# Kernel optimization log

Hardware: AMD Instinct MI355X
Metric: run time of the kernel (lower is better)

Reference implementation:

```python
import jax, jax.numpy as jnp
import numpy as np

VOCAB = 32000
EMB = 512
STATE = 512
B = 4
S = 1024


def setup_inputs() -> dict:
    key = jax.random.key(0)
    ks = jax.random.split(key, 6)
    x = jax.random.randint(ks[0], (B, S), 0, VOCAB)
    emb_table = jax.random.normal(ks[1], (VOCAB, EMB), dtype=jnp.float32)
    a = jax.random.normal(ks[2], (STATE, STATE), dtype=jnp.float32) * 0.02
    b = jax.random.normal(ks[3], (EMB, STATE), dtype=jnp.float32) * 0.02
    # nn.Linear(state, vocab): weight [vocab, state], bias [vocab]
    lim = 1.0 / np.sqrt(STATE)
    c_w = jax.random.uniform(ks[4], (VOCAB, STATE), minval=-lim, maxval=lim, dtype=jnp.float32)
    c_b = jax.random.uniform(ks[5], (VOCAB,), minval=-lim, maxval=lim, dtype=jnp.float32)
    return {"x": x, "emb_table": emb_table, "a": a, "b": b, "c_w": c_w, "c_b": c_b}


def reference(x, emb_table, a, b, c_w, c_b):
    emb = emb_table[x]                      # [B, S, E]
    # Precompute input projection for all timesteps (single GEMM).
    u = jnp.einsum('bse,en->bsn', emb, b)   # [B, S, N]
    u_t = jnp.swapaxes(u, 0, 1)             # [S, B, N] for scan

    def step(state, u_step):
        new_state = jnp.tanh(state @ a + u_step)  # [B, N]
        return new_state, new_state

    init = jnp.zeros((x.shape[0], a.shape[0]), dtype=emb.dtype)
    _, states = jax.lax.scan(step, init, u_t)   # states: [S, B, N]
    # Readout (dropout=0 -> identity). One big GEMM over all timesteps.
    logits = jnp.einsum('sbn,vn->sbv', states, c_w) + c_b  # [S, B, V]
    return jnp.swapaxes(logits, 0, 1)           # [B, S, V]
```

## Files before the change

kernel.cpp:

```cpp
#include <hip/hip_runtime.h>
#include <hip/hip_fp16.h>

typedef _Float16 f16;
typedef _Float16 f16x8 __attribute__((ext_vector_type(8)));
typedef _Float16 f16x4 __attribute__((ext_vector_type(4)));
typedef float f32x4v __attribute__((ext_vector_type(4)));

#define S_LEN 1024
#define NS 512
#define NV 32000
#define NW 4
#define SENT 0x7C007C007C007C00ULL

#define MFMA16(a, b, c) __builtin_amdgcn_mfma_f32_16x16x32_f16((a), (b), (c), 0, 0, 0)


__global__ __launch_bounds__(256) void transpose512_f16_kernel(
        const float* __restrict__ src, f16* __restrict__ dstT,
        unsigned long long* __restrict__ X) {
    int idx = blockIdx.x * 256 + threadIdx.x;
    X[idx] = SENT;
    X[idx + 262144] = SENT;
    int r = idx >> 9;
    int c = idx & 511;
    dstT[c * 512 + r] = (f16)src[idx];
}

__global__ __launch_bounds__(256) void embu_kernel(
        const int* __restrict__ x, const float* __restrict__ emb,
        const f16* __restrict__ bT, f16* __restrict__ u16) {
    __shared__ f16 embA[64 * 40];
    __shared__ f16 Bt[512 * 40];
    __shared__ int xi[64];

    int t = threadIdx.x;
    int wg = blockIdx.x;
    if (t < 64) {
        int m = wg * 64 + t;
        int bb = m & 3, ss = m >> 2;
        xi[t] = x[bb * S_LEN + ss];
    }
    __syncthreads();

    int wv = t >> 6, l = t & 63, lr = l & 15, lg = l >> 4;

    f32x4v acc[32];
#pragma unroll
    for (int i = 0; i < 32; i++) acc[i] = (f32x4v){0.f, 0.f, 0.f, 0.f};

    for (int kc = 0; kc < 512; kc += 32) {
        __syncthreads();
        {
            int tk = t >> 2, c0 = (t & 3) * 8;
            const float* src = emb + (size_t)xi[tk] * NS + kc + c0;
            float4 v0 = *(const float4*)src;
            float4 v1 = *(const float4*)(src + 4);
            f16x8 h;
            h[0] = (f16)v0.x; h[1] = (f16)v0.y; h[2] = (f16)v0.z; h[3] = (f16)v0.w;
            h[4] = (f16)v1.x; h[5] = (f16)v1.y; h[6] = (f16)v1.z; h[7] = (f16)v1.w;
            *(f16x8*)&embA[tk * 40 + c0] = h;
        }
        {
            int c0 = (t & 3) * 8;
            int n0 = t >> 2;
#pragma unroll
            for (int rr = 0; rr < 8; rr++) {
                int n = rr * 64 + n0;
                f16x8 v = *(const f16x8*)&bT[n * 512 + kc + c0];
                *(f16x8*)&Bt[n * 40 + c0] = v;
            }
        }
        __syncthreads();

        f16x8 af = *(const f16x8*)&embA[(wv * 16 + lr) * 40 + 8 * lg];
#pragma unroll
        for (int vt = 0; vt < 32; vt++) {
            f16x8 bf = *(const f16x8*)&Bt[(vt * 16 + lr) * 40 + 8 * lg];
            acc[vt] = MFMA16(af, bf, acc[vt]);
        }
    }

    int m0 = wg * 64 + wv * 16 + 4 * lg;
    int ss = m0 >> 2;
#pragma unroll
    for (int vt = 0; vt < 32; vt++) {
        int n = vt * 16 + lr;
        f16x4 h;
#pragma unroll
        for (int i = 0; i < 4; i++) h[i] = (f16)acc[vt][i];
        *(f16x4*)&u16[((size_t)ss * NS + n) * 4] = h;
    }
}

__global__ __launch_bounds__(512) void scan_kernel(
        const float* __restrict__ a, const f16* __restrict__ u16,
        f16* __restrict__ st16, unsigned long long* __restrict__ X) {
    __shared__ f16 Sb[2][4][544];

    int t = threadIdx.x;
    int r = blockIdx.x;
    int w = t >> 6, l = t & 63, lr = l & 15, lg = l >> 4;
    int col = r * 128 + w * 16 + lr;

    int gcol = -1;
    if (w < 6) {
        int cw = w + (w >= 2 * r ? 2 : 0);
        gcol = cw * 64 + l;
    }

    for (int i = t; i < 2 * 4 * 544; i += 512) ((f16*)Sb)[i] = (f16)0.f;

    f16x8 afr[16];
#pragma unroll
    for (int ks = 0; ks < 16; ks++) {
        f16x8 h;
#pragma unroll
        for (int j = 0; j < 8; j++)
            h[j] = (f16)a[(size_t)(ks * 32 + 8 * lg + j) * NS + col];
        afr[ks] = h;
    }

    f16x4 upf = *(const f16x4*)&u16[(size_t)col * 4];

    __syncthreads();

#pragma unroll 1
    for (int s = 0; s < S_LEN; s++) {
        int cur = s & 1, nxt = cur ^ 1;

        f32x4v acca, accb;
        acca[0] = (float)upf[0]; acca[1] = (float)upf[1];
        acca[2] = (float)upf[2]; acca[3] = (float)upf[3];
        accb = (f32x4v){0.f, 0.f, 0.f, 0.f};

        {
            int sn = (s + 1 < S_LEN) ? s + 1 : S_LEN - 1;
            upf = *(const f16x4*)&u16[((size_t)sn * NS + col) * 4];
        }

        const char* sb = (const char*)Sb + cur * 4352 + (lr & 3) * 1088 + lg * 16;
#pragma unroll
        for (int ks = 0; ks < 16; ks += 2) {
            f16x8 s0 = *(const f16x8*)(sb + ks * 64);
            f16x8 s1 = *(const f16x8*)(sb + ks * 64 + 64);
            acca = MFMA16(s0, afr[ks], acca);
            accb = MFMA16(s1, afr[ks + 1], accb);
        }

        if (lg == 0) {
            union { unsigned long long u; f16 h[4]; } pk;
#pragma unroll
            for (int i = 0; i < 4; i++) {
                float y = acca[i] + accb[i];
                float e = __expf(2.0f * y);
                float rc = __builtin_amdgcn_rcpf(e + 1.0f);
                y = __builtin_fmaf(-2.0f, rc, 1.0f);
                pk.h[i] = (f16)y;
            }
            __hip_atomic_store(&X[(size_t)s * NS + col], pk.u,
                               __ATOMIC_RELAXED, __HIP_MEMORY_SCOPE_AGENT);
#pragma unroll
            for (int i = 0; i < 4; i++) {
                Sb[nxt][i][col] = pk.h[i];
                st16[((size_t)s * 4 + i) * NS + col] = pk.h[i];
            }
        }

        if (s == S_LEN - 1) break;

        if (w < 6) {
            unsigned long long v;
            do {
                v = __hip_atomic_load(&X[(size_t)s * NS + gcol],
                                      __ATOMIC_RELAXED,
                                      __HIP_MEMORY_SCOPE_AGENT);
            } while (v == SENT);
            union { unsigned long long u; f16 h[4]; } pk;
            pk.u = v;
#pragma unroll
            for (int i = 0; i < 4; i++) Sb[nxt][i][gcol] = pk.h[i];
        }

        asm volatile("s_waitcnt lgkmcnt(0)" ::: "memory");
        __builtin_amdgcn_s_barrier();
        __builtin_amdgcn_sched_barrier(0);
    }
}

__global__ __launch_bounds__(512) void readout_kernel(
        const f16* __restrict__ st16, const float* __restrict__ cw,
        const float* __restrict__ cb, float* __restrict__ out) {
    __shared__ f16 Ast[256 * 72];
    __shared__ f16 Bw[128 * 72];

    int t = threadIdx.x;
    int bidx = blockIdx.x;
    int bn = bidx % 250;
    int bm = bidx / 250;
    int w = t >> 6, l = t & 63, lr = l & 15, lg = l >> 4;
    int wr = w >> 1, wc = w & 1;

    f32x4v acc[4][4];
#pragma unroll
    for (int i = 0; i < 4; i++)
#pragma unroll
        for (int j = 0; j < 4; j++) acc[i][j] = (f32x4v){0.f, 0.f, 0.f, 0.f};

    for (int kc = 0; kc < 512; kc += 64) {
        __syncthreads();
#pragma unroll
        for (int q = 0; q < 4; q++) {
            int idx = q * 512 + t;
            int row = idx >> 3;
            int c0 = (idx & 7) * 8;
            f16x8 v = *(const f16x8*)&st16[(size_t)(bm * 256 + row) * NS + kc + c0];
            *(f16x8*)&Ast[row * 72 + c0] = v;
        }
#pragma unroll
        for (int q = 0; q < 4; q++) {
            int idx = q * 512 + t;
            int row = idx >> 4;
            int c0 = (idx & 15) * 4;
            float4 v = *(const float4*)&cw[(size_t)(bn * 128 + row) * NS + kc + c0];
            f16x4 h;
            h[0] = (f16)v.x; h[1] = (f16)v.y; h[2] = (f16)v.z; h[3] = (f16)v.w;
            *(f16x4*)&Bw[row * 72 + c0] = h;
        }
        __syncthreads();

#pragma unroll
        for (int ks = 0; ks < 2; ks++) {
            f16x8 af[4], bf[4];
#pragma unroll
            for (int mt = 0; mt < 4; mt++)
                af[mt] = *(const f16x8*)&Ast[(wr * 64 + mt * 16 + lr) * 72 +
                                             ks * 32 + 8 * lg];
#pragma unroll
            for (int vt = 0; vt < 4; vt++)
                bf[vt] = *(const f16x8*)&Bw[(wc * 64 + vt * 16 + lr) * 72 +
                                            ks * 32 + 8 * lg];
#pragma unroll
            for (int mt = 0; mt < 4; mt++)
#pragma unroll
                for (int vt = 0; vt < 4; vt++)
                    acc[mt][vt] = MFMA16(af[mt], bf[vt], acc[mt][vt]);
        }
    }

    float bias[4];
#pragma unroll
    for (int vt = 0; vt < 4; vt++)
        bias[vt] = cb[bn * 128 + wc * 64 + vt * 16 + lr];

#pragma unroll
    for (int mt = 0; mt < 4; mt++) {
#pragma unroll
        for (int i = 0; i < 4; i++) {
            int m = bm * 256 + wr * 64 + mt * 16 + 4 * lg + i;
            int bb = m & 3, ss = m >> 2;
            float* orow = out + (size_t)(bb * S_LEN + ss) * NV + bn * 128 + wc * 64;
#pragma unroll
            for (int vt = 0; vt < 4; vt++)
                orow[vt * 16 + lr] = acc[mt][vt][i] + bias[vt];
        }
    }
}

extern "C" void kernel_launch(void* const* d_in, const int* in_sizes, int n_in,
                              void* d_out, int out_size, void* d_ws, size_t ws_size,
                              hipStream_t stream) {
    (void)in_sizes; (void)n_in; (void)out_size; (void)ws_size;

    const int*   x   = (const int*)d_in[0];
    const float* emb = (const float*)d_in[1];
    const float* a   = (const float*)d_in[2];
    const float* bm  = (const float*)d_in[3];
    const float* cw  = (const float*)d_in[4];
    const float* cb  = (const float*)d_in[5];
    float* out = (float*)d_out;

    char* ws = (char*)d_ws;
    f16* u16  = (f16*)(ws);
    f16* st16 = (f16*)(ws + (4u << 20));
    unsigned long long* X = (unsigned long long*)(ws + (8u << 20));
    f16* bT16 = (f16*)(ws + (12u << 20));

    transpose512_f16_kernel<<<1024, 256, 0, stream>>>(bm, bT16, X);
    embu_kernel<<<64, 256, 0, stream>>>(x, emb, bT16, u16);
    scan_kernel<<<NW, 512, 0, stream>>>(a, u16, st16, X);
    readout_kernel<<<16 * 250, 512, 0, stream>>>(st16, cw, cb, out);
}
```

Baseline: 1.498 ms.

## Fuse scan and readout into one kernel, streaming states via flags

Merges the recurrent scan and the readout GEMM into one launch. Four blocks run the scan, and the remaining blocks each wait on flag words in X until their 64-timestep slice is published, then read states directly from X. The goal is to overlap the long sequential scan with the large readout GEMM and to drop the separate st16 buffer. The cost is spinning readout blocks occupying CUs and polling memory, which may interfere with scan latency, and forward progress relies on the scan blocks being scheduled first.

```diff
diff --git a/kernel.cpp b/kernel.cpp
--- a/kernel.cpp
+++ b/kernel.cpp
@@ -5,19 +5,21 @@
 typedef _Float16 f16x8 __attribute__((ext_vector_type(8)));
 typedef _Float16 f16x4 __attribute__((ext_vector_type(4)));
 typedef float f32x4v __attribute__((ext_vector_type(4)));
+typedef unsigned long long u64;
 
 #define S_LEN 1024
 #define NS 512
 #define NV 32000
 #define NW 4
 #define SENT 0x7C007C007C007C00ULL
+#define FUSED_LDS 98304
 
 #define MFMA16(a, b, c) __builtin_amdgcn_mfma_f32_16x16x32_f16((a), (b), (c), 0, 0, 0)
 
 
 __global__ __launch_bounds__(256) void transpose512_f16_kernel(
         const float* __restrict__ src, f16* __restrict__ dstT,
-        unsigned long long* __restrict__ X) {
+        u64* __restrict__ X) {
     int idx = blockIdx.x * 256 + threadIdx.x;
     X[idx] = SENT;
     X[idx + 262144] = SENT;
@@ -92,135 +94,160 @@
     }
 }
 
-__global__ __launch_bounds__(512) void scan_kernel(
+__global__ __launch_bounds__(512) void fused_kernel(
         const float* __restrict__ a, const f16* __restrict__ u16,
-        f16* __restrict__ st16, unsigned long long* __restrict__ X) {
-    __shared__ f16 Sb[2][4][544];
-
+        const float* __restrict__ cw, const float* __restrict__ cb,
+        u64* __restrict__ X, float* __restrict__ out) {
+    extern __shared__ char smem[];
     int t = threadIdx.x;
-    int r = blockIdx.x;
+    int bid = blockIdx.x;
     int w = t >> 6, l = t & 63, lr = l & 15, lg = l >> 4;
-    int col = r * 128 + w * 16 + lr;
-
-    int gcol = -1;
-    if (w < 6) {
-        int cw = w + (w >= 2 * r ? 2 : 0);
-        gcol = cw * 64 + l;
-    }
-
-    for (int i = t; i < 2 * 4 * 544; i += 512) ((f16*)Sb)[i] = (f16)0.f;
-
-    f16x8 afr[16];
-#pragma unroll
-    for (int ks = 0; ks < 16; ks++) {
-        f16x8 h;
-#pragma unroll
-        for (int j = 0; j < 8; j++)
-            h[j] = (f16)a[(size_t)(ks * 32 + 8 * lg + j) * NS + col];
-        afr[ks] = h;
-    }
-
-    f16x4 upf = *(const f16x4*)&u16[(size_t)col * 4];
-
+
+    if (bid < NW) {
+        f16* Sb = (f16*)smem;
+        int r = bid;
+        int col = r * 128 + w * 16 + lr;
+
+        int gcol = -1;
+        if (w < 6) {
+            int cwk = w + (w >= 2 * r ? 2 : 0);
+            gcol = cwk * 64 + l;
+        }
+
+        for (int i = t; i < 2 * 4 * 544; i += 512) Sb[i] = (f16)0.f;
+
+        f16x8 afr[16];
+#pragma unroll
+        for (int ks = 0; ks < 16; ks++) {
+            f16x8 h;
+#pragma unroll
+            for (int j = 0; j < 8; j++)
+                h[j] = (f16)a[(size_t)(ks * 32 + 8 * lg + j) * NS + col];
+            afr[ks] = h;
+        }
+
+        f16x4 upf = *(const f16x4*)&u16[(size_t)col * 4];
+
+        __syncthreads();
+
+#pragma unroll 1
+        for (int s = 0; s < S_LEN; s++) {
+            int cur = s & 1, nxt = cur ^ 1;
+
+            f32x4v acca, accb;
+            acca[0] = (float)upf[0]; acca[1] = (float)upf[1];
+            acca[2] = (float)upf[2]; acca[3] = (float)upf[3];
+            accb = (f32x4v){0.f, 0.f, 0.f, 0.f};
+
+            {
+                int sn = (s + 1 < S_LEN) ? s + 1 : S_LEN - 1;
+                upf = *(const f16x4*)&u16[((size_t)sn * NS + col) * 4];
+            }
+
+            const char* sb = (const char*)Sb + cur * 4352 +
+                             (lr & 3) * 1088 + lg * 16;
+#pragma unroll
+            for (int ks = 0; ks < 16; ks += 2) {
+                f16x8 s0 = *(const f16x8*)(sb + ks * 64);
+                f16x8 s1 = *(const f16x8*)(sb + ks * 64 + 64);
+                acca = MFMA16(s0, afr[ks], acca);
+                accb = MFMA16(s1, afr[ks + 1], accb);
+            }
+
+            if (lg == 0) {
+                union { u64 u; f16 h[4]; } pk;
+#pragma unroll
+                for (int i = 0; i < 4; i++) {
+                    float y = acca[i] + accb[i];
+                    float e = __expf(2.0f * y);
+                    float rc = __builtin_amdgcn_rcpf(e + 1.0f);
+                    y = __builtin_fmaf(-2.0f, rc, 1.0f);
+                    pk.h[i] = (f16)y;
+                }
+                __hip_atomic_store(&X[(size_t)s * NS + col], pk.u,
+                                   __ATOMIC_RELAXED, __HIP_MEMORY_SCOPE_AGENT);
+#pragma unroll
+                for (int i = 0; i < 4; i++)
+                    Sb[nxt * 2176 + i * 544 + col] = pk.h[i];
+            }
+
+            if (s == S_LEN - 1) break;
+
+            if (w < 6) {
+                u64 v;
+                do {
+                    v = __hip_atomic_load(&X[(size_t)s * NS + gcol],
+                                          __ATOMIC_RELAXED,
+                                          __HIP_MEMORY_SCOPE_AGENT);
+                } while (v == SENT);
+                union { u64 u; f16 h[4]; } pk;
+                pk.u = v;
+#pragma unroll
+                for (int i = 0; i < 4; i++)
+                    Sb[nxt * 2176 + i * 544 + gcol] = pk.h[i];
+            }
+
+            asm volatile("s_waitcnt lgkmcnt(0)" ::: "memory");
+            __builtin_amdgcn_s_barrier();
+            __builtin_amdgcn_sched_barrier(0);
+        }
+        return;
+    }
+
+    f16* Ast = (f16*)smem;
+    f16* Bw = (f16*)(smem + 256 * 72 * 2);
+
+    int idx = bid - NW;
+    int bm = idx / 250;
+    int bn = idx % 250;
+    int s0 = bm * 64;
+
+    if (t == 0) {
+        int sc = (bm == 15) ? (S_LEN - 1) : (s0 + 64);
+        while (__hip_atomic_load(&X[(size_t)sc * NS], __ATOMIC_RELAXED,
+                                 __HIP_MEMORY_SCOPE_AGENT) == SENT)
+            __builtin_amdgcn_s_sleep(16);
+    }
     __syncthreads();
 
-#pragma unroll 1
-    for (int s = 0; s < S_LEN; s++) {
-        int cur = s & 1, nxt = cur ^ 1;
-
-        f32x4v acca, accb;
-        acca[0] = (float)upf[0]; acca[1] = (float)upf[1];
-        acca[2] = (float)upf[2]; acca[3] = (float)upf[3];
-        accb = (f32x4v){0.f, 0.f, 0.f, 0.f};
-
+    int wr = w >> 1, wc = w & 1;
+
+    f32x4v acc[4][4];
+#pragma unroll
+    for (int i = 0; i < 4; i++)
+#pragma unroll
+        for (int j = 0; j < 4; j++) acc[i][j] = (f32x4v){0.f, 0.f, 0.f, 0.f};
+
+    for (int kc = 0; kc < 512; kc += 64) {
+        __syncthreads();
         {
-            int sn = (s + 1 < S_LEN) ? s + 1 : S_LEN - 1;
-            upf = *(const f16x4*)&u16[((size_t)sn * NS + col) * 4];
-        }
-
-        const char* sb = (const char*)Sb + cur * 4352 + (lr & 3) * 1088 + lg * 16;
-#pragma unroll
-        for (int ks = 0; ks < 16; ks += 2) {
-            f16x8 s0 = *(const f16x8*)(sb + ks * 64);
-            f16x8 s1 = *(const f16x8*)(sb + ks * 64 + 64);
-            acca = MFMA16(s0, afr[ks], acca);
-            accb = MFMA16(s1, afr[ks + 1], accb);
-        }
-
-        if (lg == 0) {
-            union { unsigned long long u; f16 h[4]; } pk;
-#pragma unroll
-            for (int i = 0; i < 4; i++) {
-                float y = acca[i] + accb[i];
-                float e = __expf(2.0f * y);
-                float rc = __builtin_amdgcn_rcpf(e + 1.0f);
-                y = __builtin_fmaf(-2.0f, rc, 1.0f);
-                pk.h[i] = (f16)y;
-            }
-            __hip_atomic_store(&X[(size_t)s * NS + col], pk.u,
-                               __ATOMIC_RELAXED, __HIP_MEMORY_SCOPE_AGENT);
-#pragma unroll
-            for (int i = 0; i < 4; i++) {
-                Sb[nxt][i][col] = pk.h[i];
-                st16[((size_t)s * 4 + i) * NS + col] = pk.h[i];
-            }
-        }
-
-        if (s == S_LEN - 1) break;
-
-        if (w < 6) {
-            unsigned long long v;
-            do {
-                v = __hip_atomic_load(&X[(size_t)s * NS + gcol],
-                                      __ATOMIC_RELAXED,
-                                      __HIP_MEMORY_SCOPE_AGENT);
-            } while (v == SENT);
-            union { unsigned long long u; f16 h[4]; } pk;
-            pk.u = v;
-#pragma unroll
-            for (int i = 0; i < 4; i++) Sb[nxt][i][gcol] = pk.h[i];
-        }
-
-        asm volatile("s_waitcnt lgkmcnt(0)" ::: "memory");
-        __builtin_amdgcn_s_barrier();
-        __builtin_amdgcn_sched_barrier(0);
-    }
-}
-
-__global__ __launch_bounds__(512) void readout_kernel(
-        const f16* __restrict__ st16, const float* __restrict__ cw,
-        const float* __restrict__ cb, float* __restrict__ out) {
-    __shared__ f16 Ast[256 * 72];
-    __shared__ f16 Bw[128 * 72];
-
-    int t = threadIdx.x;
-    int bidx = blockIdx.x;
-    int bn = bidx % 250;
-    int bm = bidx / 250;
-    int w = t >> 6, l = t & 63, lr = l & 15, lg = l >> 4;
-    int wr = w >> 1, wc = w & 1;
-
-    f32x4v acc[4][4];
-#pragma unroll
-    for (int i = 0; i < 4; i++)
-#pragma unroll
-        for (int j = 0; j < 4; j++) acc[i][j] = (f32x4v){0.f, 0.f, 0.f, 0.f};
-
-    for (int kc = 0; kc < 512; kc += 64) {
-        __syncthreads();
+            int srel = t >> 3;
+            int ck = (t & 7) * 8;
+            const u64* xs = &X[(size_t)(s0 + srel) * NS + kc + ck];
+            u64 v[8];
+#pragma unroll
+            for (int j = 0; j < 8; j++)
+                v[j] = __hip_atomic_load(&xs[j], __ATOMIC_RELAXED,
+                                         __HIP_MEMORY_SCOPE_AGENT);
+#pragma unroll
+            for (int j = 0; j < 8; j++)
+                while (v[j] == SENT)
+                    v[j] = __hip_atomic_load(&xs[j], __ATOMIC_RELAXED,
+                                             __HIP_MEMORY_SCOPE_AGENT);
+#pragma unroll
+            for (int j = 0; j < 8; j++) {
+                union { u64 u; f16 h[4]; } pk;
+                pk.u = v[j];
+#pragma unroll
+                for (int b = 0; b < 4; b++)
+                    Ast[(srel * 4 + b) * 72 + ck + j] = pk.h[b];
+            }
+        }
 #pragma unroll
         for (int q = 0; q < 4; q++) {
-            int idx = q * 512 + t;
-            int row = idx >> 3;
-            int c0 = (idx & 7) * 8;
-            f16x8 v = *(const f16x8*)&st16[(size_t)(bm * 256 + row) * NS + kc + c0];
-            *(f16x8*)&Ast[row * 72 + c0] = v;
-        }
-#pragma unroll
-        for (int q = 0; q < 4; q++) {
-            int idx = q * 512 + t;
-            int row = idx >> 4;
-            int c0 = (idx & 15) * 4;
+            int i2 = q * 512 + t;
+            int row = i2 >> 4;
+            int c0 = (i2 & 15) * 4;
             float4 v = *(const float4*)&cw[(size_t)(bn * 128 + row) * NS + kc + c0];
             f16x4 h;
             h[0] = (f16)v.x; h[1] = (f16)v.y; h[2] = (f16)v.z; h[3] = (f16)v.w;
@@ -280,13 +307,16 @@
     float* out = (float*)d_out;
 
     char* ws = (char*)d_ws;
-    f16* u16  = (f16*)(ws);
-    f16* st16 = (f16*)(ws + (4u << 20));
-    unsigned long long* X = (unsigned long long*)(ws + (8u << 20));
-    f16* bT16 = (f16*)(ws + (12u << 20));
+    f16* u16 = (f16*)(ws);
+    u64* X   = (u64*)(ws + (4u << 20));
+    f16* bT16 = (f16*)(ws + (8u << 20));
+
+    hipFuncSetAttribute(reinterpret_cast<const void*>(fused_kernel),
+                        hipFuncAttributeMaxDynamicSharedMemorySize,
+                        FUSED_LDS);
 
     transpose512_f16_kernel<<<1024, 256, 0, stream>>>(bm, bT16, X);
     embu_kernel<<<64, 256, 0, stream>>>(x, emb, bT16, u16);
-    scan_kernel<<<NW, 512, 0, stream>>>(a, u16, st16, X);
-    readout_kernel<<<16 * 250, 512, 0, stream>>>(st16, cw, cb, out);
+    fused_kernel<<<NW + 16 * 250, 512, FUSED_LDS, stream>>>(
+        a, u16, cw, cb, X, out);
 }
```

After: 1.351 ms. 9.8% less time.
